# Performance work log

Measured on AMD Instinct MI355X. Metric: run time of the kernel, lower is better.

The kernel has to match this reference:

```python
import jax, jax.numpy as jnp
import numpy as np

N = 2048          # num agents / graph nodes
D = 128           # n_actor == n_map
ALPHA = 0.2       # GAT leakyrelu alpha
NEG = -1e9
X_IDX = [4, 9, 14, 19]   # actors_inter_cat time indices per LSTM step
E_IDX = [0, 4, 9, 14]    # graph_adjs time indices per LSTM step


def setup_inputs() -> dict:
    key = jax.random.key(0)
    ks = jax.random.split(key, 10)
    xavier = lambda k, shape: jax.random.uniform(
        k, shape, jnp.float32, -1.0, 1.0) * 1.414 * np.sqrt(6.0 / (shape[-2] + shape[-1]))
    actors_inter_cat = jax.random.normal(ks[0], (N, 20, D), jnp.float32)
    graph_adjs = jax.random.randint(ks[1], (N, 20, N), 0, 2, jnp.int32)
    # 4 GAT_SRF gates (forget, input, input_cell, output), stacked on leading axis
    Wg = xavier(ks[2], (4, 2 * D, D))          # gate projection W: in=2*D, out=D
    ag = xavier(ks[3], (4, 2 * D))             # attention vector a (2*out_features,)
    W = xavier(ks[4], (D, D))                  # GAT cell output projection
    b = xavier(ks[5], (1, D))
    h0 = xavier(ks[6], (1, D))
    conv_w = jax.random.normal(ks[7], (3, D, D, 2), jnp.float32) * (1.0 / np.sqrt(2 * D))
    conv_b = jax.random.normal(ks[8], (3, D), jnp.float32) * 0.01
    return {"actors_inter_cat": actors_inter_cat, "graph_adjs": graph_adjs,
            "Wg": Wg, "ag": ag, "W": W, "b": b, "h0": h0,
            "conv_w": conv_w, "conv_b": conv_b}


def _gat_gates(gin, mask, Wg, ag):
    # gin: (N, 2D); mask: (N, N) bool. Computes all 4 GAT_SRF gates at once.
    Wh = jnp.einsum('nf,gfo->gno', gin, Wg)                 # (4, N, D)
    s_src = jnp.einsum('gno,go->gn', Wh, ag[:, :D])         # a^T [Wh_i ..]
    s_dst = jnp.einsum('gno,go->gn', Wh, ag[:, D:])
    e = jax.nn.leaky_relu(s_src[:, :, None] + s_dst[:, None, :], ALPHA)  # (4,N,N)
    e = jnp.where(mask[None], e, NEG)
    attn = jax.nn.softmax(e, axis=-1)
    return jax.nn.elu(jnp.einsum('gnm,gmo->gno', attn, Wh))  # concat=True -> ELU


def reference(actors_inter_cat, graph_adjs, Wg, ag, W, b, h0, conv_w, conv_b):
    n = actors_inter_cat.shape[0]
    cell = actors_inter_cat[:, 0, :]
    hidden = jnp.broadcast_to(h0, (n, D))
    outs = []
    for t in range(4):  # fixed 4-step recurrence
        X = actors_inter_cat[:, X_IDX[t], :]
        mask = graph_adjs[:, E_IDX[t], :] > 0
        gin = jnp.concatenate([X, hidden], axis=1)          # (N, 2D)
        g = _gat_gates(gin, mask, Wg, ag)                   # (4, N, D)
        forget = jax.nn.sigmoid(g[0])
        inp_gate = jax.nn.sigmoid(g[1])
        inp_cell = jnp.tanh(g[2])
        out_gate = jax.nn.sigmoid(g[3])
        cell = cell * forget + inp_gate * inp_cell
        hidden = jnp.tanh(cell) * out_gate
        outs.append(jax.nn.sigmoid(hidden @ W + b))
    y = jnp.stack(outs, axis=2)                             # (N, D, 4)
    for l in range(3):  # kernel-2 Conv1d stack: length 4 -> 3 -> 2 -> 1
        y = (jnp.einsum('nct,oc->not', y[:, :, :-1], conv_w[l, :, :, 0])
             + jnp.einsum('nct,oc->not', y[:, :, 1:], conv_w[l, :, :, 1])
             + conv_b[l][None, :, None])
    return y[:, :, 0]                                       # squeeze -> (N, D)
```

## Files before the change

### kernel.cpp

```cpp
#include <hip/hip_runtime.h>

typedef __attribute__((ext_vector_type(8))) short short8;
typedef __attribute__((ext_vector_type(4))) float floatx4;

#define MFMA16(a,b,c) __builtin_amdgcn_mfma_f32_16x16x32_bf16(a,b,c,0,0,0)

__device__ __forceinline__ unsigned short f2bf(float f){
  unsigned u = __float_as_uint(f);
  u += 0x7fffu + ((u >> 16) & 1u);
  return (unsigned short)(u >> 16);
}
__device__ __forceinline__ float sigm(float x){ return 1.f/(1.f+__expf(-x)); }

__global__ __launch_bounds__(256) void prep_kernel(const float* __restrict__ actors,
    const float* __restrict__ h0, const float* __restrict__ Wg, const float* __restrict__ cw,
    const int* __restrict__ adj, unsigned short* __restrict__ hbf, float* __restrict__ cell,
    unsigned short* __restrict__ WgT, float* __restrict__ cwT, unsigned long long* __restrict__ bm){
  int bid = blockIdx.x;
  if (bid < 1024){
    int idx = bid*256 + threadIdx.x;
    int n = idx >> 7, c = idx & 127;
    hbf[idx]  = f2bf(h0[c]);
    cell[idx] = actors[(size_t)n*2560 + c];
  } else if (bid < 1536){
    int e = (bid-1024)*256 + threadIdx.x;
    int g = e >> 15, o = (e >> 8) & 127, f = e & 255;
    WgT[(size_t)g*32768 + o*256 + f] = f2bf(Wg[(size_t)g*32768 + f*128 + o]);
  } else if (bid < 1728){
    int e = (bid-1536)*256 + threadIdx.x;
    int l = e >> 14, rr = e & 16383, k = rr >> 7, o = rr & 127;
    cwT[(size_t)l*32768 + k*256 + o]       = cw[(size_t)l*32768 + o*256 + k*2];
    cwT[(size_t)l*32768 + k*256 + 128 + o] = cw[(size_t)l*32768 + o*256 + k*2 + 1];
  } else {
    const int E[4] = {0,4,9,14};
    int mb = bid - 1728;
    int t = mb & 3, nblk = mb >> 2;
    int wv = threadIdx.x >> 6, lane = threadIdx.x & 63;
    int n = nblk*4 + wv;
    const int* row = adj + (size_t)n*40960 + (size_t)E[t]*2048;
    unsigned long long* outp = bm + ((size_t)t*2048 + n)*32;
    for (int it=0; it<32; ++it){
      unsigned long long bal = __ballot(row[it*64 + lane] > 0);
      if (lane == 0) outp[it] = bal;
    }
  }
}

__global__ __launch_bounds__(256) void whgemm_kernel(const float* __restrict__ actors,
    const unsigned short* __restrict__ hbf, const unsigned short* __restrict__ WgT,
    const float* __restrict__ ag, unsigned short* __restrict__ WhT,
    float* __restrict__ s_src, float* __restrict__ s_dst, int xoff){
  __shared__ __align__(16) unsigned short ginb[32*264];
  __shared__ float sred[4][2][32];
  int g = blockIdx.y, n0 = blockIdx.x*32, tid = threadIdx.x;
  {
    int row = tid >> 3, q = tid & 7;
    if (q < 4){
      const float4* src = (const float4*)(actors + (size_t)(n0+row)*2560 + xoff + q*32);
      unsigned short* dst = &ginb[row*264 + q*32];
      #pragma unroll
      for (int j=0;j<4;++j){
        float4 a = src[2*j], b = src[2*j+1];
        unsigned short tmp[8] = {f2bf(a.x),f2bf(a.y),f2bf(a.z),f2bf(a.w),
                                 f2bf(b.x),f2bf(b.y),f2bf(b.z),f2bf(b.w)};
        *(uint4*)(dst + j*8) = *(const uint4*)tmp;
      }
    } else {
      const uint4* src = (const uint4*)(hbf + (size_t)(n0+row)*128 + (q-4)*32);
      uint4* dst = (uint4*)&ginb[row*264 + 128 + (q-4)*32];
      #pragma unroll
      for (int j=0;j<4;++j) dst[j] = src[j];
    }
  }
  __syncthreads();
  int wv = tid>>6, lane = tid&63, quad = lane>>4, l16 = lane&15;
  int ob = wv*32;
  floatx4 acc[2][2];
  #pragma unroll
  for (int i=0;i<2;++i) for (int j=0;j<2;++j) acc[i][j] = (floatx4){0.f,0.f,0.f,0.f};
  const unsigned short* wga = WgT + (size_t)g*32768;
  #pragma unroll
  for (int kh=0; kh<8; ++kh){
    int k = kh*32 + quad*8;
    short8 a0 = *(const short8*)(wga + (size_t)(ob + l16)*256 + k);
    short8 a1 = *(const short8*)(wga + (size_t)(ob + 16 + l16)*256 + k);
    #pragma unroll
    for (int j=0;j<2;++j){
      short8 b = *(const short8*)&ginb[(j*16 + l16)*264 + k];
      acc[0][j] = MFMA16(a0, b, acc[0][j]);
      acc[1][j] = MFMA16(a1, b, acc[1][j]);
    }
  }
  float agS[2][4], agD[2][4];
  #pragma unroll
  for (int i=0;i<2;++i)
    #pragma unroll
    for (int r=0;r<4;++r){
      int o = ob + i*16 + quad*4 + r;
      agS[i][r] = ag[g*256 + o];
      agD[i][r] = ag[g*256 + 128 + o];
    }
  unsigned short* wht = WhT + (size_t)g*262144;
  float psrc[2], pdst[2];
  #pragma unroll
  for (int j=0;j<2;++j){
    float ps = 0.f, pd = 0.f;
    #pragma unroll
    for (int i=0;i<2;++i)
      #pragma unroll
      for (int r=0;r<4;++r){
        float v = acc[i][j][r];
        ps += v*agS[i][r]; pd += v*agD[i][r];
        wht[(size_t)(ob + i*16 + quad*4 + r)*2048 + n0 + j*16 + l16] = f2bf(v);
      }
    psrc[j] = ps; pdst[j] = pd;
  }
  #pragma unroll
  for (int j=0;j<2;++j){
    psrc[j] += __shfl_down(psrc[j], 16); psrc[j] += __shfl_down(psrc[j], 32);
    pdst[j] += __shfl_down(pdst[j], 16); pdst[j] += __shfl_down(pdst[j], 32);
  }
  if (quad == 0){
    #pragma unroll
    for (int j=0;j<2;++j){
      sred[wv][0][j*16+l16] = psrc[j];
      sred[wv][1][j*16+l16] = pdst[j];
    }
  }
  __syncthreads();
  if (tid < 64){
    int which = tid>>5, n = tid&31;
    float s = sred[0][which][n]+sred[1][which][n]+sred[2][which][n]+sred[3][which][n];
    (which ? s_dst : s_src)[g*2048 + n0 + n] = s;
  }
}

__global__ __launch_bounds__(512) void attn_kernel(const unsigned char* __restrict__ bmb,
    const unsigned short* __restrict__ WhT, const float* __restrict__ s_src,
    const float* __restrict__ s_dst, float* __restrict__ gout, int t){
  __shared__ float obuf[2][2][16][72];
  __shared__ float zpart[4][16];
  __shared__ float zrow[16];
  int g = blockIdx.y, n0 = blockIdx.x*16, tid = threadIdx.x;
  int w = tid>>6, lane = tid&63, quad = lane>>4, l16 = lane&15;
  int ohalf = w & 1, mg = w >> 1;
  const unsigned short* whg = WhT + (size_t)g*262144 + (size_t)(ohalf*64)*2048;
  const float* sd = s_dst + g*2048;
  float srcv = s_src[g*2048 + n0 + l16];
  const unsigned char* mr = bmb + ((size_t)t*2048 + n0 + l16)*256;
  float z0 = 0.f;
  floatx4 acc[4];
  #pragma unroll
  for (int j=0;j<4;++j) acc[j] = (floatx4){0.f,0.f,0.f,0.f};
  for (int c=0;c<8;++c){
    int mbase = mg*512 + c*64;
    #pragma unroll
    for (int kh=0; kh<2; ++kh){
      int mk = mbase + kh*32 + quad*8;
      float4 sda = *(const float4*)(sd + mk);
      float4 sdb = *(const float4*)(sd + mk + 4);
      unsigned mb = mr[mk>>3];
      float sv[8] = {sda.x,sda.y,sda.z,sda.w,sdb.x,sdb.y,sdb.z,sdb.w};
      short8 a0;
      #pragma unroll
      for (int j=0;j<8;++j){
        float s = srcv + sv[j];
        s = s > 0.f ? s : 0.2f*s;
        float p = ((mb >> j) & 1u) ? __expf(s) : 0.f;
        z0 += p;
        a0[j] = (short)f2bf(p);
      }
      const unsigned short* bp = whg + mk;
      #pragma unroll
      for (int j=0;j<4;++j){
        short8 b = *(const short8*)(bp + (size_t)(j*16 + l16)*2048);
        acc[j] = MFMA16(a0, b, acc[j]);
      }
    }
  }
  z0 += __shfl_down(z0, 32);
  z0 += __shfl_down(z0, 16);
  if (ohalf == 0 && lane < 16) zpart[mg][l16] = z0;
  if (mg < 2){
    #pragma unroll
    for (int j=0;j<4;++j)
      #pragma unroll
      for (int r=0;r<4;++r)
        obuf[ohalf][mg][quad*4+r][j*16+l16] = acc[j][r];
  }
  __syncthreads();
  if (mg >= 2){
    #pragma unroll
    for (int j=0;j<4;++j)
      #pragma unroll
      for (int r=0;r<4;++r)
        obuf[ohalf][mg-2][quad*4+r][j*16+l16] += acc[j][r];
  }
  if (tid < 16) zrow[tid] = zpart[0][tid]+zpart[1][tid]+zpart[2][tid]+zpart[3][tid];
  __syncthreads();
  {
    int row = tid>>5, c0 = (tid&31)*4;
    int half = c0>>6, oc = c0&63;
    float inv = 1.f / zrow[row];
    float* go = gout + (size_t)g*262144 + (size_t)(n0+row)*128 + c0;
    #pragma unroll
    for (int j=0;j<4;++j){
      float v = (obuf[half][0][row][oc+j] + obuf[half][1][row][oc+j]) * inv;
      go[j] = v > 0.f ? v : __expf(v) - 1.f;
    }
  }
}

__global__ __launch_bounds__(256) void gate_kernel(const float* __restrict__ gbuf,
    float* __restrict__ cell, unsigned short* __restrict__ hbf, const float* __restrict__ W,
    const float* __restrict__ b, float* __restrict__ y, int t){
  __shared__ float h[256];
  int tid = threadIdx.x;
  int r = tid >> 7, o = tid & 127;
  int n = blockIdx.x*2 + r;
  size_t idx = (size_t)n*128 + o;
  float g0 = gbuf[idx], g1 = gbuf[262144+idx], g2 = gbuf[524288+idx], g3 = gbuf[786432+idx];
  float fg = sigm(g0), ig = sigm(g1), ic = tanhf(g2), og = sigm(g3);
  float cl = cell[idx]*fg + ig*ic;
  float hd = tanhf(cl)*og;
  cell[idx] = cl; hbf[idx] = f2bf(hd);
  h[tid] = hd;
  __syncthreads();
  float acc = b[o];
  const float* hr = h + r*128;
  for (int k=0;k<128;++k) acc += hr[k]*W[k*128+o];
  y[(size_t)n*512 + o*4 + t] = sigm(acc);
}

__global__ __launch_bounds__(256) void convfused_kernel(const float* __restrict__ yin,
    const float* __restrict__ cwT, const float* __restrict__ cb, float* __restrict__ out){
  __shared__ float ylds[2][128][4];
  int tid = threadIdx.x;
  int r = tid >> 7, o = tid & 127;
  int n = blockIdx.x*2 + r;
  *(float4*)&ylds[r][o][0] = *(const float4*)&yin[(size_t)n*512 + o*4];
  __syncthreads();
  {
    const float* w = cwT;
    float a0=0.f, a1=0.f, a2=0.f;
    for (int k=0;k<128;++k){
      float w0 = w[k*256 + o], w1 = w[k*256 + 128 + o];
      float y0 = ylds[r][k][0], y1 = ylds[r][k][1], y2 = ylds[r][k][2], y3 = ylds[r][k][3];
      a0 += y0*w0 + y1*w1; a1 += y1*w0 + y2*w1; a2 += y2*w0 + y3*w1;
    }
    float bb = cb[o];
    __syncthreads();
    ylds[r][o][0] = a0+bb; ylds[r][o][1] = a1+bb; ylds[r][o][2] = a2+bb;
    __syncthreads();
  }
  {
    const float* w = cwT + 32768;
    float a0=0.f, a1=0.f;
    for (int k=0;k<128;++k){
      float w0 = w[k*256 + o], w1 = w[k*256 + 128 + o];
      float y0 = ylds[r][k][0], y1 = ylds[r][k][1], y2 = ylds[r][k][2];
      a0 += y0*w0 + y1*w1; a1 += y1*w0 + y2*w1;
    }
    float bb = cb[128 + o];
    __syncthreads();
    ylds[r][o][0] = a0+bb; ylds[r][o][1] = a1+bb;
    __syncthreads();
  }
  {
    const float* w = cwT + 65536;
    float a0=0.f;
    for (int k=0;k<128;++k){
      float w0 = w[k*256 + o], w1 = w[k*256 + 128 + o];
      a0 += ylds[r][k][0]*w0 + ylds[r][k][1]*w1;
    }
    out[(size_t)n*128 + o] = a0 + cb[256 + o];
  }
}

extern "C" void kernel_launch(void* const* d_in, const int* in_sizes, int n_in,
                              void* d_out, int out_size, void* d_ws, size_t ws_size,
                              hipStream_t stream) {
  const float* actors = (const float*)d_in[0];
  const int*   adj    = (const int*)d_in[1];
  const float* Wg     = (const float*)d_in[2];
  const float* ag     = (const float*)d_in[3];
  const float* W      = (const float*)d_in[4];
  const float* b      = (const float*)d_in[5];
  const float* h0     = (const float*)d_in[6];
  const float* cw     = (const float*)d_in[7];
  const float* cb     = (const float*)d_in[8];
  float* out = (float*)d_out;

  char* ws = (char*)d_ws;
  unsigned long long* bm = (unsigned long long*)ws;
  float* cell          = (float*)(ws + (size_t)(2u<<20));
  unsigned short* hbf  = (unsigned short*)(ws + (size_t)(3u<<20));
  unsigned short* WgT  = (unsigned short*)(ws + (size_t)3670016);
  float* s_src         = (float*)(ws + (size_t)3932160);
  float* s_dst         = (float*)(ws + (size_t)3932160 + 32768);
  unsigned short* WhT  = (unsigned short*)(ws + (size_t)(4u<<20));
  float* cwT           = (float*)(ws + (size_t)(6u<<20));
  float* gbuf          = (float*)(ws + (size_t)(7u<<20));
  float* yA            = (float*)(ws + (size_t)(11u<<20));

  const int XI[4] = {4, 9, 14, 19};

  prep_kernel<<<3776, 256, 0, stream>>>(actors, h0, Wg, cw, adj, hbf, cell, WgT, cwT, bm);
  for (int t=0; t<4; ++t){
    whgemm_kernel<<<dim3(64,4), 256, 0, stream>>>(actors, hbf, WgT, ag, WhT, s_src, s_dst, XI[t]*128);
    attn_kernel  <<<dim3(128,4), 512, 0, stream>>>((const unsigned char*)bm, WhT, s_src, s_dst, gbuf, t);
    gate_kernel  <<<1024, 256, 0, stream>>>(gbuf, cell, hbf, W, b, yA, t);
  }
  convfused_kernel<<<1024, 256, 0, stream>>>(yA, cwT, cb, out);
}
```

Before: 674.5 us.

## Fuse gate update into Wh GEMM and conv tail, pre-tile Wg/Wh for MFMA

The LSTM gate update and output projection move into the next step's Wh GEMM kernel, and the last step's gate update moves into the conv stack kernel. This removes one launch per step and the bf16 hidden-state round trip. Wg and Wh are stored in MFMA-fragment tiled layouts so each lane does contiguous 16-byte loads. The attention kernel drops to 256 threads, with each wave covering all 128 outputs over a quarter of the neighbours and loading its mask bits once up front. The fused GEMM kernel runs only 128 blocks and loops over the 4 gates serially, so occupancy there is lower.

Result: faster. 622.2 us (-7.8%).

```diff
diff --git a/kernel.cpp b/kernel.cpp
--- a/kernel.cpp
+++ b/kernel.cpp
@@ -12,20 +12,22 @@
 }
 __device__ __forceinline__ float sigm(float x){ return 1.f/(1.f+__expf(-x)); }
 
+
 __global__ __launch_bounds__(256) void prep_kernel(const float* __restrict__ actors,
-    const float* __restrict__ h0, const float* __restrict__ Wg, const float* __restrict__ cw,
-    const int* __restrict__ adj, unsigned short* __restrict__ hbf, float* __restrict__ cell,
-    unsigned short* __restrict__ WgT, float* __restrict__ cwT, unsigned long long* __restrict__ bm){
+    const float* __restrict__ Wg, const float* __restrict__ cw, const int* __restrict__ adj,
+    float* __restrict__ cell, unsigned short* __restrict__ WgA, float* __restrict__ cwT,
+    unsigned long long* __restrict__ bm){
   int bid = blockIdx.x;
   if (bid < 1024){
     int idx = bid*256 + threadIdx.x;
     int n = idx >> 7, c = idx & 127;
-    hbf[idx]  = f2bf(h0[c]);
     cell[idx] = actors[(size_t)n*2560 + c];
   } else if (bid < 1536){
     int e = (bid-1024)*256 + threadIdx.x;
-    int g = e >> 15, o = (e >> 8) & 127, f = e & 255;
-    WgT[(size_t)g*32768 + o*256 + f] = f2bf(Wg[(size_t)g*32768 + f*128 + o]);
+    int g = e >> 15, o = (e >> 8) & 127, k = e & 255;
+    unsigned short v = f2bf(Wg[(size_t)g*32768 + k*128 + o]);
+    int off = ((o>>4)*8 + (k>>5))*512 + (((k>>3)&3)*16 + (o&15))*8 + (k&7);
+    WgA[(size_t)g*32768 + off] = v;
   } else if (bid < 1728){
     int e = (bid-1536)*256 + threadIdx.x;
     int l = e >> 14, rr = e & 16383, k = rr >> 7, o = rr & 127;
@@ -46,199 +48,211 @@
   }
 }
 
-__global__ __launch_bounds__(256) void whgemm_kernel(const float* __restrict__ actors,
-    const unsigned short* __restrict__ hbf, const unsigned short* __restrict__ WgT,
-    const float* __restrict__ ag, unsigned short* __restrict__ WhT,
-    float* __restrict__ s_src, float* __restrict__ s_dst, int xoff){
-  __shared__ __align__(16) unsigned short ginb[32*264];
-  __shared__ float sred[4][2][32];
-  int g = blockIdx.y, n0 = blockIdx.x*32, tid = threadIdx.x;
-  {
-    int row = tid >> 3, q = tid & 7;
-    if (q < 4){
-      const float4* src = (const float4*)(actors + (size_t)(n0+row)*2560 + xoff + q*32);
-      unsigned short* dst = &ginb[row*264 + q*32];
-      #pragma unroll
-      for (int j=0;j<4;++j){
-        float4 a = src[2*j], b = src[2*j+1];
-        unsigned short tmp[8] = {f2bf(a.x),f2bf(a.y),f2bf(a.z),f2bf(a.w),
-                                 f2bf(b.x),f2bf(b.y),f2bf(b.z),f2bf(b.w)};
-        *(uint4*)(dst + j*8) = *(const uint4*)tmp;
-      }
-    } else {
-      const uint4* src = (const uint4*)(hbf + (size_t)(n0+row)*128 + (q-4)*32);
-      uint4* dst = (uint4*)&ginb[row*264 + 128 + (q-4)*32];
-      #pragma unroll
-      for (int j=0;j<4;++j) dst[j] = src[j];
-    }
-  }
-  __syncthreads();
-  int wv = tid>>6, lane = tid&63, quad = lane>>4, l16 = lane&15;
-  int ob = wv*32;
-  floatx4 acc[2][2];
-  #pragma unroll
-  for (int i=0;i<2;++i) for (int j=0;j<2;++j) acc[i][j] = (floatx4){0.f,0.f,0.f,0.f};
-  const unsigned short* wga = WgT + (size_t)g*32768;
-  #pragma unroll
-  for (int kh=0; kh<8; ++kh){
-    int k = kh*32 + quad*8;
-    short8 a0 = *(const short8*)(wga + (size_t)(ob + l16)*256 + k);
-    short8 a1 = *(const short8*)(wga + (size_t)(ob + 16 + l16)*256 + k);
-    #pragma unroll
-    for (int j=0;j<2;++j){
-      short8 b = *(const short8*)&ginb[(j*16 + l16)*264 + k];
-      acc[0][j] = MFMA16(a0, b, acc[0][j]);
-      acc[1][j] = MFMA16(a1, b, acc[1][j]);
-    }
-  }
-  float agS[2][4], agD[2][4];
-  #pragma unroll
-  for (int i=0;i<2;++i)
-    #pragma unroll
-    for (int r=0;r<4;++r){
-      int o = ob + i*16 + quad*4 + r;
-      agS[i][r] = ag[g*256 + o];
-      agD[i][r] = ag[g*256 + 128 + o];
-    }
-  unsigned short* wht = WhT + (size_t)g*262144;
-  float psrc[2], pdst[2];
-  #pragma unroll
-  for (int j=0;j<2;++j){
+__global__ __launch_bounds__(256) void gatewh_kernel(const float* __restrict__ actors,
+    const float* __restrict__ gbuf, float* __restrict__ cell, const float* __restrict__ h0,
+    const float* __restrict__ W, const float* __restrict__ bvec,
+    const unsigned short* __restrict__ WgA, const float* __restrict__ ag,
+    float* __restrict__ y, unsigned short* __restrict__ WhB,
+    float* __restrict__ s_src, float* __restrict__ s_dst, int xoff, int t){
+  __shared__ float hl[16][132];
+  __shared__ __align__(16) unsigned short ginb[16*264];
+  __shared__ float sredS[4][4][16], sredD[4][4][16];
+  int n0 = blockIdx.x*16, tid = threadIdx.x;
+  int row = tid>>4, o0 = (tid&15)*8;
+  if (t == 0){
+    const float* hp = h0 + o0;
+    #pragma unroll
+    for (int j=0;j<8;++j) hl[row][o0+j] = hp[j];
+  } else {
+    size_t idx = (size_t)(n0+row)*128 + o0;
+    float4 ga0 = *(const float4*)(gbuf+idx),          ga1 = *(const float4*)(gbuf+idx+4);
+    float4 gb0 = *(const float4*)(gbuf+262144+idx),   gb1 = *(const float4*)(gbuf+262144+idx+4);
+    float4 gc0 = *(const float4*)(gbuf+524288+idx),   gc1 = *(const float4*)(gbuf+524288+idx+4);
+    float4 gd0 = *(const float4*)(gbuf+786432+idx),   gd1 = *(const float4*)(gbuf+786432+idx+4);
+    float4 c0 = *(const float4*)(cell+idx),           c1 = *(const float4*)(cell+idx+4);
+    float fgv[8] = {ga0.x,ga0.y,ga0.z,ga0.w,ga1.x,ga1.y,ga1.z,ga1.w};
+    float igv[8] = {gb0.x,gb0.y,gb0.z,gb0.w,gb1.x,gb1.y,gb1.z,gb1.w};
+    float icv[8] = {gc0.x,gc0.y,gc0.z,gc0.w,gc1.x,gc1.y,gc1.z,gc1.w};
+    float ogv[8] = {gd0.x,gd0.y,gd0.z,gd0.w,gd1.x,gd1.y,gd1.z,gd1.w};
+    float cv[8]  = {c0.x,c0.y,c0.z,c0.w,c1.x,c1.y,c1.z,c1.w};
+    float cl[8], hd[8];
+    #pragma unroll
+    for (int j=0;j<8;++j){
+      cl[j] = cv[j]*sigm(fgv[j]) + sigm(igv[j])*tanhf(icv[j]);
+      hd[j] = tanhf(cl[j])*sigm(ogv[j]);
+      hl[row][o0+j] = hd[j];
+    }
+    *(float4*)(cell+idx)   = (float4){cl[0],cl[1],cl[2],cl[3]};
+    *(float4*)(cell+idx+4) = (float4){cl[4],cl[5],cl[6],cl[7]};
+  }
+  __syncthreads();
+  if (t >= 1){
+    float acc[8];
+    float4 b0 = *(const float4*)(bvec+o0), b1 = *(const float4*)(bvec+o0+4);
+    acc[0]=b0.x;acc[1]=b0.y;acc[2]=b0.z;acc[3]=b0.w;acc[4]=b1.x;acc[5]=b1.y;acc[6]=b1.z;acc[7]=b1.w;
+    for (int k=0;k<128;++k){
+      float hv = hl[row][k];
+      float4 w0 = *(const float4*)(W + (size_t)k*128 + o0);
+      float4 w1 = *(const float4*)(W + (size_t)k*128 + o0 + 4);
+      acc[0]+=hv*w0.x; acc[1]+=hv*w0.y; acc[2]+=hv*w0.z; acc[3]+=hv*w0.w;
+      acc[4]+=hv*w1.x; acc[5]+=hv*w1.y; acc[6]+=hv*w1.z; acc[7]+=hv*w1.w;
+    }
+    float* yp = y + (size_t)(t-1)*262144 + (size_t)(n0+row)*128 + o0;
+    #pragma unroll
+    for (int j=0;j<8;++j) yp[j] = sigm(acc[j]);
+  }
+  {
+    const float* ap = actors + (size_t)(n0+row)*2560 + xoff + o0;
+    float4 a = *(const float4*)ap, bb = *(const float4*)(ap+4);
+    unsigned short tmp[8] = {f2bf(a.x),f2bf(a.y),f2bf(a.z),f2bf(a.w),
+                             f2bf(bb.x),f2bf(bb.y),f2bf(bb.z),f2bf(bb.w)};
+    *(uint4*)&ginb[row*264 + o0] = *(const uint4*)tmp;
+    unsigned short tmp2[8];
+    #pragma unroll
+    for (int j=0;j<8;++j) tmp2[j] = f2bf(hl[row][o0+j]);
+    *(uint4*)&ginb[row*264 + 128 + o0] = *(const uint4*)tmp2;
+  }
+  __syncthreads();
+  int w = tid>>6, lane = tid&63, quad = lane>>4, l16 = lane&15;
+  int m32 = blockIdx.x>>1, min32 = (blockIdx.x&1)*16 + l16;
+  int qp = min32>>3, jp = min32&7;
+  for (int g=0; g<4; ++g){
+    floatx4 acc0 = {0.f,0.f,0.f,0.f}, acc1 = acc0;
+    const unsigned short* wa = WgA + (size_t)g*32768;
+    #pragma unroll
+    for (int kh=0; kh<8; ++kh){
+      short8 bfr = *(const short8*)&ginb[l16*264 + kh*32 + quad*8];
+      short8 a0 = *(const short8*)(wa + (size_t)(((w*2+0)*8 + kh)*64 + lane)*8);
+      short8 a1 = *(const short8*)(wa + (size_t)(((w*2+1)*8 + kh)*64 + lane)*8);
+      acc0 = MFMA16(a0, bfr, acc0);
+      acc1 = MFMA16(a1, bfr, acc1);
+    }
     float ps = 0.f, pd = 0.f;
-    #pragma unroll
-    for (int i=0;i<2;++i)
+    unsigned short* wb = WhB + (size_t)(g*8 + w*2)*32768 + m32*512 + qp*128 + jp;
+    const float* agp = ag + g*256;
+    #pragma unroll
+    for (int i=0;i<2;++i){
+      floatx4 ac = i ? acc1 : acc0;
       #pragma unroll
       for (int r=0;r<4;++r){
-        float v = acc[i][j][r];
-        ps += v*agS[i][r]; pd += v*agD[i][r];
-        wht[(size_t)(ob + i*16 + quad*4 + r)*2048 + n0 + j*16 + l16] = f2bf(v);
+        int o = w*32 + i*16 + quad*4 + r;
+        float v = ac[r];
+        ps += v*agp[o]; pd += v*agp[128+o];
+        wb[i*32768 + (quad*4+r)*8] = f2bf(v);
       }
-    psrc[j] = ps; pdst[j] = pd;
-  }
-  #pragma unroll
-  for (int j=0;j<2;++j){
-    psrc[j] += __shfl_down(psrc[j], 16); psrc[j] += __shfl_down(psrc[j], 32);
-    pdst[j] += __shfl_down(pdst[j], 16); pdst[j] += __shfl_down(pdst[j], 32);
-  }
-  if (quad == 0){
-    #pragma unroll
-    for (int j=0;j<2;++j){
-      sred[wv][0][j*16+l16] = psrc[j];
-      sred[wv][1][j*16+l16] = pdst[j];
-    }
-  }
-  __syncthreads();
-  if (tid < 64){
-    int which = tid>>5, n = tid&31;
-    float s = sred[0][which][n]+sred[1][which][n]+sred[2][which][n]+sred[3][which][n];
+    }
+    ps += __shfl_down(ps,32); ps += __shfl_down(ps,16);
+    pd += __shfl_down(pd,32); pd += __shfl_down(pd,16);
+    if (lane < 16){ sredS[g][w][l16] = ps; sredD[g][w][l16] = pd; }
+  }
+  __syncthreads();
+  if (tid < 128){
+    int g = tid>>5, which = (tid>>4)&1, n = tid&15;
+    float s;
+    if (which) s = sredD[g][0][n]+sredD[g][1][n]+sredD[g][2][n]+sredD[g][3][n];
+    else       s = sredS[g][0][n]+sredS[g][1][n]+sredS[g][2][n]+sredS[g][3][n];
     (which ? s_dst : s_src)[g*2048 + n0 + n] = s;
   }
 }
 
-__global__ __launch_bounds__(512) void attn_kernel(const unsigned char* __restrict__ bmb,
-    const unsigned short* __restrict__ WhT, const float* __restrict__ s_src,
+__global__ __launch_bounds__(256) void attn_kernel(const unsigned char* __restrict__ bmb,
+    const unsigned short* __restrict__ WhB, const float* __restrict__ s_src,
     const float* __restrict__ s_dst, float* __restrict__ gout, int t){
-  __shared__ float obuf[2][2][16][72];
+  __shared__ float obuf[2][16][132];
   __shared__ float zpart[4][16];
-  __shared__ float zrow[16];
   int g = blockIdx.y, n0 = blockIdx.x*16, tid = threadIdx.x;
   int w = tid>>6, lane = tid&63, quad = lane>>4, l16 = lane&15;
-  int ohalf = w & 1, mg = w >> 1;
-  const unsigned short* whg = WhT + (size_t)g*262144 + (size_t)(ohalf*64)*2048;
+  float srcv = s_src[g*2048 + n0 + l16];
   const float* sd = s_dst + g*2048;
-  float srcv = s_src[g*2048 + n0 + l16];
-  const unsigned char* mr = bmb + ((size_t)t*2048 + n0 + l16)*256;
+  const unsigned char* mrow = bmb + ((size_t)t*2048 + n0 + l16)*256 + w*64;
+  uint4 mq0 = *(const uint4*)mrow,      mq1 = *(const uint4*)(mrow+16);
+  uint4 mq2 = *(const uint4*)(mrow+32), mq3 = *(const uint4*)(mrow+48);
+  unsigned mwd[16] = {mq0.x,mq0.y,mq0.z,mq0.w, mq1.x,mq1.y,mq1.z,mq1.w,
+                      mq2.x,mq2.y,mq2.z,mq2.w, mq3.x,mq3.y,mq3.z,mq3.w};
+  const unsigned short* wb = WhB + (size_t)g*262144;
   float z0 = 0.f;
-  floatx4 acc[4];
+  floatx4 acc[8];
   #pragma unroll
-  for (int j=0;j<4;++j) acc[j] = (floatx4){0.f,0.f,0.f,0.f};
-  for (int c=0;c<8;++c){
-    int mbase = mg*512 + c*64;
-    #pragma unroll
-    for (int kh=0; kh<2; ++kh){
-      int mk = mbase + kh*32 + quad*8;
-      float4 sda = *(const float4*)(sd + mk);
-      float4 sdb = *(const float4*)(sd + mk + 4);
-      unsigned mb = mr[mk>>3];
-      float sv[8] = {sda.x,sda.y,sda.z,sda.w,sdb.x,sdb.y,sdb.z,sdb.w};
-      short8 a0;
-      #pragma unroll
-      for (int j=0;j<8;++j){
-        float s = srcv + sv[j];
-        s = s > 0.f ? s : 0.2f*s;
-        float p = ((mb >> j) & 1u) ? __expf(s) : 0.f;
-        z0 += p;
-        a0[j] = (short)f2bf(p);
-      }
-      const unsigned short* bp = whg + mk;
-      #pragma unroll
-      for (int j=0;j<4;++j){
-        short8 b = *(const short8*)(bp + (size_t)(j*16 + l16)*2048);
-        acc[j] = MFMA16(a0, b, acc[j]);
-      }
-    }
-  }
-  z0 += __shfl_down(z0, 32);
-  z0 += __shfl_down(z0, 16);
-  if (ohalf == 0 && lane < 16) zpart[mg][l16] = z0;
-  if (mg < 2){
-    #pragma unroll
-    for (int j=0;j<4;++j)
+  for (int j=0;j<8;++j) acc[j] = (floatx4){0.f,0.f,0.f,0.f};
+  #pragma unroll
+  for (int c=0; c<16; ++c){
+    int mk = w*512 + c*32 + quad*8;
+    float4 sa = *(const float4*)(sd + mk);
+    float4 sb = *(const float4*)(sd + mk + 4);
+    unsigned mb = (mwd[c] >> (quad*8)) & 0xffu;
+    float sv[8] = {sa.x,sa.y,sa.z,sa.w,sb.x,sb.y,sb.z,sb.w};
+    short8 a0;
+    #pragma unroll
+    for (int j=0;j<8;++j){
+      float s = srcv + sv[j];
+      s = s > 0.f ? s : 0.2f*s;
+      float p = ((mb >> j) & 1u) ? __expf(s) : 0.f;
+      z0 += p;
+      a0[j] = (short)f2bf(p);
+    }
+    const unsigned short* bp = wb + (size_t)(w*16 + c)*512 + lane*8;
+    #pragma unroll
+    for (int o16=0; o16<8; ++o16){
+      short8 bfr = *(const short8*)(bp + (size_t)o16*32768);
+      acc[o16] = MFMA16(a0, bfr, acc[o16]);
+    }
+  }
+  z0 += __shfl_down(z0,32); z0 += __shfl_down(z0,16);
+  if (lane < 16) zpart[w][l16] = z0;
+  if (w < 2){
+    #pragma unroll
+    for (int o16=0;o16<8;++o16)
       #pragma unroll
       for (int r=0;r<4;++r)
-        obuf[ohalf][mg][quad*4+r][j*16+l16] = acc[j][r];
-  }
-  __syncthreads();
-  if (mg >= 2){
-    #pragma unroll
-    for (int j=0;j<4;++j)
+        obuf[w][quad*4+r][o16*16+l16] = acc[o16][r];
+  }
+  __syncthreads();
+  if (w >= 2){
+    #pragma unroll
+    for (int o16=0;o16<8;++o16)
       #pragma unroll
       for (int r=0;r<4;++r)
-        obuf[ohalf][mg-2][quad*4+r][j*16+l16] += acc[j][r];
-  }
-  if (tid < 16) zrow[tid] = zpart[0][tid]+zpart[1][tid]+zpart[2][tid]+zpart[3][tid];
-  __syncthreads();
-  {
-    int row = tid>>5, c0 = (tid&31)*4;
-    int half = c0>>6, oc = c0&63;
-    float inv = 1.f / zrow[row];
+        obuf[w-2][quad*4+r][o16*16+l16] += acc[o16][r];
+  }
+  __syncthreads();
+  {
+    int row = tid>>4, c0 = (tid&15)*8;
+    float z = zpart[0][row]+zpart[1][row]+zpart[2][row]+zpart[3][row];
+    float inv = 1.f / z;
     float* go = gout + (size_t)g*262144 + (size_t)(n0+row)*128 + c0;
     #pragma unroll
-    for (int j=0;j<4;++j){
-      float v = (obuf[half][0][row][oc+j] + obuf[half][1][row][oc+j]) * inv;
+    for (int j=0;j<8;++j){
+      float v = (obuf[0][row][c0+j] + obuf[1][row][c0+j]) * inv;
       go[j] = v > 0.f ? v : __expf(v) - 1.f;
     }
   }
 }
 
-__global__ __launch_bounds__(256) void gate_kernel(const float* __restrict__ gbuf,
-    float* __restrict__ cell, unsigned short* __restrict__ hbf, const float* __restrict__ W,
-    const float* __restrict__ b, float* __restrict__ y, int t){
-  __shared__ float h[256];
+__global__ __launch_bounds__(256) void convgate_kernel(const float* __restrict__ gbuf,
+    const float* __restrict__ cell, const float* __restrict__ W, const float* __restrict__ bvec,
+    const float* __restrict__ y, const float* __restrict__ cwT, const float* __restrict__ cb,
+    float* __restrict__ out){
+  __shared__ float hl[2][128];
+  __shared__ float ylds[2][128][4];
   int tid = threadIdx.x;
   int r = tid >> 7, o = tid & 127;
   int n = blockIdx.x*2 + r;
   size_t idx = (size_t)n*128 + o;
-  float g0 = gbuf[idx], g1 = gbuf[262144+idx], g2 = gbuf[524288+idx], g3 = gbuf[786432+idx];
-  float fg = sigm(g0), ig = sigm(g1), ic = tanhf(g2), og = sigm(g3);
-  float cl = cell[idx]*fg + ig*ic;
-  float hd = tanhf(cl)*og;
-  cell[idx] = cl; hbf[idx] = f2bf(hd);
-  h[tid] = hd;
-  __syncthreads();
-  float acc = b[o];
-  const float* hr = h + r*128;
-  for (int k=0;k<128;++k) acc += hr[k]*W[k*128+o];
-  y[(size_t)n*512 + o*4 + t] = sigm(acc);
-}
-
-__global__ __launch_bounds__(256) void convfused_kernel(const float* __restrict__ yin,
-    const float* __restrict__ cwT, const float* __restrict__ cb, float* __restrict__ out){
-  __shared__ float ylds[2][128][4];
-  int tid = threadIdx.x;
-  int r = tid >> 7, o = tid & 127;
-  int n = blockIdx.x*2 + r;
-  *(float4*)&ylds[r][o][0] = *(const float4*)&yin[(size_t)n*512 + o*4];
+  {
+    float g0 = gbuf[idx], g1 = gbuf[262144+idx], g2 = gbuf[524288+idx], g3 = gbuf[786432+idx];
+    float cl = cell[idx]*sigm(g0) + sigm(g1)*tanhf(g2);
+    hl[r][o] = tanhf(cl)*sigm(g3);
+  }
+  ylds[r][o][0] = y[idx];
+  ylds[r][o][1] = y[262144+idx];
+  ylds[r][o][2] = y[524288+idx];
+  __syncthreads();
+  {
+    float acc = bvec[o];
+    const float* hr = hl[r];
+    for (int k=0;k<128;++k) acc += hr[k]*W[(size_t)k*128+o];
+    ylds[r][o][3] = sigm(acc);
+  }
   __syncthreads();
   {
     const float* w = cwT;
@@ -273,7 +287,7 @@
       float w0 = w[k*256 + o], w1 = w[k*256 + 128 + o];
       a0 += ylds[r][k][0]*w0 + ylds[r][k][1]*w1;
     }
-    out[(size_t)n*128 + o] = a0 + cb[256 + o];
+    out[idx] = a0 + cb[256 + o];
   }
 }
 
@@ -294,22 +308,22 @@
   char* ws = (char*)d_ws;
   unsigned long long* bm = (unsigned long long*)ws;
   float* cell          = (float*)(ws + (size_t)(2u<<20));
-  unsigned short* hbf  = (unsigned short*)(ws + (size_t)(3u<<20));
-  unsigned short* WgT  = (unsigned short*)(ws + (size_t)3670016);
+  unsigned short* WgA  = (unsigned short*)(ws + (size_t)(3u<<20));
+  float* cwT           = (float*)(ws + (size_t)3407872);
   float* s_src         = (float*)(ws + (size_t)3932160);
   float* s_dst         = (float*)(ws + (size_t)3932160 + 32768);
-  unsigned short* WhT  = (unsigned short*)(ws + (size_t)(4u<<20));
-  float* cwT           = (float*)(ws + (size_t)(6u<<20));
+  unsigned short* WhB  = (unsigned short*)(ws + (size_t)(4u<<20));
   float* gbuf          = (float*)(ws + (size_t)(7u<<20));
-  float* yA            = (float*)(ws + (size_t)(11u<<20));
+  float* yplanes       = (float*)(ws + (size_t)(11u<<20));
 
   const int XI[4] = {4, 9, 14, 19};
 
-  prep_kernel<<<3776, 256, 0, stream>>>(actors, h0, Wg, cw, adj, hbf, cell, WgT, cwT, bm);
+  prep_kernel<<<3776, 256, 0, stream>>>(actors, Wg, cw, adj, cell, WgA, cwT, bm);
   for (int t=0; t<4; ++t){
-    whgemm_kernel<<<dim3(64,4), 256, 0, stream>>>(actors, hbf, WgT, ag, WhT, s_src, s_dst, XI[t]*128);
-    attn_kernel  <<<dim3(128,4), 512, 0, stream>>>((const unsigned char*)bm, WhT, s_src, s_dst, gbuf, t);
-    gate_kernel  <<<1024, 256, 0, stream>>>(gbuf, cell, hbf, W, b, yA, t);
-  }
-  convfused_kernel<<<1024, 256, 0, stream>>>(yA, cwT, cb, out);
-}
+    gatewh_kernel<<<128, 256, 0, stream>>>(actors, gbuf, cell, h0, W, b, WgA, ag,
+                                           yplanes, WhB, s_src, s_dst, XI[t]*128, t);
+    attn_kernel<<<dim3(128,4), 256, 0, stream>>>((const unsigned char*)bm, WhB,
+                                                 s_src, s_dst, gbuf, t);
+  }
+  convgate_kernel<<<1024, 256, 0, stream>>>(gbuf, cell, W, b, yplanes, cwT, cb, out);
+}
```
